# Kernel optimization log

Measured on AMD Instinct MI355X. Metric: run time of the kernel, lower is better.

The kernel has to match this reference:

```python
import jax, jax.numpy as jnp
import numpy as np

N = 50000      # nodes
E = 600000     # edges
F_IN = 9       # atom features
H = 128        # hidden dim
G = 2048       # graphs in batch
EPS = 1e-5     # batchnorm eps


def setup_inputs() -> dict:
    key = jax.random.key(0)
    ks = jax.random.split(key, 24)

    def lin(k, i, o):
        return (jax.random.normal(k, (i, o), jnp.float32) / np.sqrt(i).astype(np.float32))

    x = jax.random.normal(ks[0], (N, F_IN), jnp.float32)
    edge_index = jax.random.randint(ks[1], (2, E), 0, N, dtype=jnp.int32)
    # deterministic sorted graph assignment: every graph non-empty (~24 nodes each)
    batch = ((jnp.arange(N, dtype=jnp.int32) * G) // N).astype(jnp.int32)

    return {
        "x": x, "edge_index": edge_index, "batch": batch,
        "W0": lin(ks[2], F_IN, H), "b0": jnp.zeros((H,), jnp.float32),
        "g0": jnp.ones((H,), jnp.float32), "be0": jnp.zeros((H,), jnp.float32),
        "W1": lin(ks[3], H, H), "b1": jnp.zeros((H,), jnp.float32),
        "g1": jnp.ones((H,), jnp.float32), "be1": jnp.zeros((H,), jnp.float32),
        "W2": lin(ks[4], H, H), "b2": jnp.zeros((H,), jnp.float32),
        "g2": jnp.ones((H,), jnp.float32), "be2": jnp.zeros((H,), jnp.float32),
        "fc1_w": lin(ks[5], 2 * H, H), "fc1_b": jnp.zeros((H,), jnp.float32),
        "fc2_w": lin(ks[6], H, H // 2), "fc2_b": jnp.zeros((H // 2,), jnp.float32),
        "out_w": lin(ks[7], H // 2, 5), "out_b": jnp.zeros((5,), jnp.float32),
    }


def _gcn_conv(x, src, dst, W, b):
    # PyG GCNConv: add self-loops, symmetric deg^-1/2 normalization.
    h = x @ W                                   # [N, H_out]
    deg = jax.ops.segment_sum(jnp.ones((E,), h.dtype), dst, num_segments=N) + 1.0
    dis = jax.lax.rsqrt(deg)                    # deg^-1/2 incl. self-loop
    coef = dis[src] * dis[dst]                  # [E]
    agg = jax.ops.segment_sum(h[src] * coef[:, None], dst, num_segments=N)
    agg = agg + h * (dis * dis)[:, None]        # self-loop messages
    return agg + b


def _bn_relu(x, g, b):
    m = jnp.mean(x, axis=0)
    v = jnp.mean(jnp.square(x - m), axis=0)     # biased variance (torch BN)
    return jax.nn.relu((x - m) * jax.lax.rsqrt(v + EPS) * g + b)


def reference(x, edge_index, batch,
              W0, b0, g0, be0, W1, b1, g1, be1, W2, b2, g2, be2,
              fc1_w, fc1_b, fc2_w, fc2_b, out_w, out_b):
    src, dst = edge_index[0], edge_index[1]

    h = _bn_relu(_gcn_conv(x, src, dst, W0, b0), g0, be0)
    h = _bn_relu(_gcn_conv(h, src, dst, W1, b1), g1, be1)
    h = _bn_relu(_gcn_conv(h, src, dst, W2, b2), g2, be2)

    counts = jax.ops.segment_sum(jnp.ones((N,), h.dtype), batch, num_segments=G)
    x_mean = jax.ops.segment_sum(h, batch, num_segments=G) / jnp.maximum(counts, 1.0)[:, None]
    x_max = jax.ops.segment_max(h, batch, num_segments=G)

    z = jnp.concatenate([x_mean, x_max], axis=1)        # [G, 2H]
    z = jax.nn.relu(z @ fc1_w + fc1_b)
    z = jax.nn.relu(z @ fc2_w + fc2_b)
    return z @ out_w + out_b                            # [G, 5]
```

## Files before the change

### kernel.cpp

```cpp
#include <hip/hip_runtime.h>
#include <hip/hip_bf16.h>

#define N_NODES 50000
#define N_EDGES 600000
#define F_INX 9
#define HD 128
#define G_GRAPHS 2048
#define BN_EPS 1e-5f

#define SCAN_CHUNK 1024
#define SCAN_BLOCKS ((N_NODES + SCAN_CHUNK - 1) / SCAN_CHUNK)
#define BN_SLICES 16
#define BN_LAYER_F (BN_SLICES * 256)

typedef __bf16 bf16x8 __attribute__((ext_vector_type(8)));
typedef float f32x4 __attribute__((ext_vector_type(4)));

__device__ inline unsigned short f2bf(float f) {
    union { float f; unsigned u; } v;
    v.f = f;
    unsigned r = v.u + 0x7fff + ((v.u >> 16) & 1);
    return (unsigned short)(r >> 16);
}
__device__ inline float asf(unsigned u) {
    union { unsigned u; float f; } v;
    v.u = u;
    return v.f;
}

__global__ void k_zero(int* __restrict__ cnt, float* __restrict__ bnacc) {
    int i = blockIdx.x * blockDim.x + threadIdx.x;
    if (i < N_NODES) cnt[i] = 0;
    if (i < 3 * BN_LAYER_F) bnacc[i] = 0.0f;
}

__global__ void k_count(const int* __restrict__ dst, int* __restrict__ cnt) {
    int e = blockIdx.x * blockDim.x + threadIdx.x;
    if (e < N_EDGES) atomicAdd(&cnt[dst[e]], 1);
}

__global__ void k_scanA(const int* __restrict__ cnt, int* __restrict__ blocksum) {
    __shared__ int red[256];
    int b = blockIdx.x, t = threadIdx.x;
    int idx = b * SCAN_CHUNK + t * 4;
    int s = 0;
    if (idx + 3 < N_NODES) {
        int4 v = *(const int4*)(cnt + idx);
        s = v.x + v.y + v.z + v.w;
    }
    red[t] = s;
    __syncthreads();
    for (int off = 128; off > 0; off >>= 1) {
        if (t < off) red[t] += red[t + off];
        __syncthreads();
    }
    if (t == 0) blocksum[b] = red[0];
}

__global__ void k_scanB(const int* __restrict__ blocksum, int* __restrict__ blockoff) {
    int t = threadIdx.x;
    int v = (t < SCAN_BLOCKS) ? blocksum[t] : 0;
    int incl = v;
    for (int off = 1; off < 64; off <<= 1) {
        int u = __shfl_up(incl, off, 64);
        if (t >= off) incl += u;
    }
    if (t < SCAN_BLOCKS) blockoff[t] = incl - v;
}

__global__ void k_scanC(const int* __restrict__ cnt, const int* __restrict__ blockoff,
                        int* __restrict__ rowptr, int* __restrict__ cursor,
                        float* __restrict__ dis) {
    __shared__ int pre[256];
    int b = blockIdx.x, t = threadIdx.x;
    int idx = b * SCAN_CHUNK + t * 4;
    int4 v = make_int4(0, 0, 0, 0);
    bool valid = (idx + 3 < N_NODES);
    if (valid) v = *(const int4*)(cnt + idx);
    int s = v.x + v.y + v.z + v.w;
    pre[t] = s;
    __syncthreads();
    for (int off = 1; off < 256; off <<= 1) {
        int u = (t >= off) ? pre[t - off] : 0;
        __syncthreads();
        pre[t] += u;
        __syncthreads();
    }
    if (valid) {
        int base = blockoff[b] + pre[t] - s;
        int4 rp;
        rp.x = base;
        rp.y = base + v.x;
        rp.z = rp.y + v.y;
        rp.w = rp.z + v.z;
        *(int4*)(rowptr + idx) = rp;
        *(int4*)(cursor + idx) = rp;
        float4 dv = make_float4(rsqrtf((float)v.x + 1.0f), rsqrtf((float)v.y + 1.0f),
                                rsqrtf((float)v.z + 1.0f), rsqrtf((float)v.w + 1.0f));
        *(float4*)(dis + idx) = dv;
    }
}

__global__ void k_scatter(const int* __restrict__ src, const int* __restrict__ dst,
                          const float* __restrict__ dis, int* __restrict__ cursor,
                          unsigned* __restrict__ ebuf) {
    int e = blockIdx.x * blockDim.x + threadIdx.x;
    if (e >= N_EDGES) return;
    int s = src[e], d = dst[e];
    int pos = atomicAdd(&cursor[d], 1);
    float coef = dis[s] * dis[d];
    ebuf[pos] = (unsigned)(s & 0xffff) | ((unsigned)f2bf(coef) << 16);
}

__global__ void k_wconv(const float* __restrict__ W, unsigned short* __restrict__ Wt) {
    int i = blockIdx.x * blockDim.x + threadIdx.x;
    int k = i >> 7, n = i & 127;
    Wt[n * HD + k] = f2bf(W[k * HD + n]);
}

template <int K, int NPB>
__global__ void k_lin0(const float* __restrict__ in, const float* __restrict__ W,
                       unsigned short* __restrict__ hout) {
    __shared__ float rows[NPB][K];
    int node0 = blockIdx.x * NPB;
    int c = threadIdx.x;
    for (int i = c; i < NPB * K; i += HD) {
        int n = i / K, k = i % K;
        int node = node0 + n;
        rows[n][k] = (node < N_NODES) ? in[(size_t)node * K + k] : 0.0f;
    }
    __syncthreads();
    float acc[NPB];
#pragma unroll
    for (int n = 0; n < NPB; ++n) acc[n] = 0.0f;
#pragma unroll
    for (int k = 0; k < K; ++k) {
        float w = W[k * HD + c];
#pragma unroll
        for (int n = 0; n < NPB; ++n) acc[n] += rows[n][k] * w;
    }
#pragma unroll
    for (int n = 0; n < NPB; ++n) {
        int node = node0 + n;
        if (node < N_NODES) hout[(size_t)node * HD + c] = f2bf(acc[n]);
    }
}

#define LIN_ROWS 64
#define ATS 136

__global__ __launch_bounds__(256, 3) void k_linear_mfma(
        const float* __restrict__ in, const unsigned short* __restrict__ Wt,
        const float* __restrict__ bnp,
        const float* __restrict__ gam, const float* __restrict__ bet,
        unsigned short* __restrict__ hout) {
    __shared__ __align__(16) unsigned short At[LIN_ROWS][ATS];
    __shared__ __align__(16) unsigned short Bt[HD][ATS];
    __shared__ float sc_s[HD], sh_s[HD];
    int node0 = blockIdx.x * LIN_ROWS;
    int t = threadIdx.x;

    if (t < HD) {
        float s = 0.0f, q = 0.0f;
#pragma unroll
        for (int i = 0; i < BN_SLICES; ++i) {
            s += bnp[i * 256 + t];
            q += bnp[i * 256 + 128 + t];
        }
        const float inv_n = 1.0f / (float)N_NODES;
        float m = s * inv_n;
        float v = q * inv_n - m * m;
        float sc = gam[t] * rsqrtf(v + BN_EPS);
        sc_s[t] = sc;
        sh_s[t] = bet[t] - m * sc;
    }
    __syncthreads();

    for (int i = t; i < LIN_ROWS * 32; i += 256) {
        int r = i >> 5;
        int k4 = (i & 31) * 4;
        int node = node0 + r;
        float4 v = make_float4(0.f, 0.f, 0.f, 0.f);
        if (node < N_NODES) v = *(const float4*)(in + (size_t)node * HD + k4);
        ushort4 o;
        o.x = f2bf(fmaxf(0.f, v.x * sc_s[k4 + 0] + sh_s[k4 + 0]));
        o.y = f2bf(fmaxf(0.f, v.y * sc_s[k4 + 1] + sh_s[k4 + 1]));
        o.z = f2bf(fmaxf(0.f, v.z * sc_s[k4 + 2] + sh_s[k4 + 2]));
        o.w = f2bf(fmaxf(0.f, v.w * sc_s[k4 + 3] + sh_s[k4 + 3]));
        *(ushort4*)&At[r][k4] = o;
    }
    for (int c = t; c < HD * 16; c += 256) {
        int n = c >> 4, k8 = (c & 15) * 8;
        *(ushort4*)&Bt[n][k8] = *(const ushort4*)(Wt + (size_t)n * HD + k8);
        *(ushort4*)&Bt[n][k8 + 4] = *(const ushort4*)(Wt + (size_t)n * HD + k8 + 4);
    }
    __syncthreads();

    int w = t >> 6, l = t & 63;
    int quad = l >> 4, lc = l & 15;
    int arow = w * 16 + lc;
    int koff = quad * 8;

    f32x4 acc[8];
#pragma unroll
    for (int nt = 0; nt < 8; ++nt) acc[nt] = (f32x4){0.f, 0.f, 0.f, 0.f};

#pragma unroll
    for (int kb = 0; kb < HD; kb += 32) {
        bf16x8 af = *(const bf16x8*)&At[arow][kb + koff];
#pragma unroll
        for (int nt = 0; nt < 8; ++nt) {
            bf16x8 bfg = *(const bf16x8*)&Bt[nt * 16 + lc][kb + koff];
            acc[nt] = __builtin_amdgcn_mfma_f32_16x16x32_bf16(af, bfg, acc[nt], 0, 0, 0);
        }
    }

    int node_base = node0 + w * 16 + quad * 4;
#pragma unroll
    for (int nt = 0; nt < 8; ++nt) {
#pragma unroll
        for (int r = 0; r < 4; ++r) {
            int node = node_base + r;
            if (node < N_NODES)
                hout[(size_t)node * HD + nt * 16 + lc] = f2bf(acc[nt][r]);
        }
    }
}

__global__ __launch_bounds__(256, 8) void k_gather(
        const int* __restrict__ rowptr, const int* __restrict__ cnt,
        const unsigned* __restrict__ ebuf, const unsigned short* __restrict__ h,
        const float* __restrict__ dis, float* __restrict__ agg,
        float* __restrict__ bnp) {
    __shared__ float redS[4][256];
    __shared__ float redQ[4][256];
    int wv = threadIdx.x >> 6;
    int lane = threadIdx.x & 63;
    int node = __builtin_amdgcn_readfirstlane(blockIdx.x * 4 + wv);
    const unsigned* h32 = (const unsigned*)h;

    int start = rowptr[node];
    int deg = cnt[node];
    float d = dis[node];
    unsigned sv = h32[(size_t)node * 64 + lane];
    float dd = d * d;
    float acc0 = asf(sv << 16) * dd;
    float acc1 = asf(sv & 0xffff0000u) * dd;

    int e = start, end = start + deg;
    for (; e + 4 <= end; e += 4) {
        unsigned r0 = ebuf[e], r1 = ebuf[e + 1], r2 = ebuf[e + 2], r3 = ebuf[e + 3];
        unsigned hv0 = h32[(size_t)(r0 & 0xffffu) * 64 + lane];
        unsigned hv1 = h32[(size_t)(r1 & 0xffffu) * 64 + lane];
        unsigned hv2 = h32[(size_t)(r2 & 0xffffu) * 64 + lane];
        unsigned hv3 = h32[(size_t)(r3 & 0xffffu) * 64 + lane];
        float c0 = asf(r0 & 0xffff0000u), c1 = asf(r1 & 0xffff0000u);
        float c2 = asf(r2 & 0xffff0000u), c3 = asf(r3 & 0xffff0000u);
        acc0 += asf(hv0 << 16) * c0;
        acc1 += asf(hv0 & 0xffff0000u) * c0;
        acc0 += asf(hv1 << 16) * c1;
        acc1 += asf(hv1 & 0xffff0000u) * c1;
        acc0 += asf(hv2 << 16) * c2;
        acc1 += asf(hv2 & 0xffff0000u) * c2;
        acc0 += asf(hv3 << 16) * c3;
        acc1 += asf(hv3 & 0xffff0000u) * c3;
    }
    for (; e < end; ++e) {
        unsigned r = ebuf[e];
        unsigned hv = h32[(size_t)(r & 0xffffu) * 64 + lane];
        float cf = asf(r & 0xffff0000u);
        acc0 += asf(hv << 16) * cf;
        acc1 += asf(hv & 0xffff0000u) * cf;
    }

    ((float2*)agg)[(size_t)node * 64 + lane] = make_float2(acc0, acc1);

    redS[wv][2 * lane] = acc0;
    redS[wv][2 * lane + 1] = acc1;
    redQ[wv][2 * lane] = acc0 * acc0;
    redQ[wv][2 * lane + 1] = acc1 * acc1;
    __syncthreads();
    int t = threadIdx.x;
    int ch = t & 127;
    int which = t >> 7;
    float val;
    if (which == 0)
        val = redS[0][ch] + redS[1][ch] + redS[2][ch] + redS[3][ch];
    else
        val = redQ[0][ch] + redQ[1][ch] + redQ[2][ch] + redQ[3][ch];
    int slice = blockIdx.x & (BN_SLICES - 1);
    atomicAdd(&bnp[slice * 256 + which * 128 + ch], val);
}

__global__ void k_head(const float* __restrict__ agg, const float* __restrict__ bnp,
                       const float* __restrict__ gam, const float* __restrict__ bet,
                       const float* __restrict__ fc1_w, const float* __restrict__ fc1_b,
                       const float* __restrict__ fc2_w, const float* __restrict__ fc2_b,
                       const float* __restrict__ out_w, const float* __restrict__ out_b,
                       float* __restrict__ out) {
    __shared__ float z[2 * HD];
    __shared__ float z1[HD];
    __shared__ float z2[64];
    int g = blockIdx.x, c = threadIdx.x;
    float s = 0.0f, q = 0.0f;
#pragma unroll
    for (int i = 0; i < BN_SLICES; ++i) {
        s += bnp[i * 256 + c];
        q += bnp[i * 256 + 128 + c];
    }
    const float inv_n = 1.0f / (float)N_NODES;
    float m = s * inv_n;
    float v = q * inv_n - m * m;
    float sc = gam[c] * rsqrtf(v + BN_EPS);
    float sh = bet[c] - m * sc;
    int start = (g * N_NODES + G_GRAPHS - 1) / G_GRAPHS;
    int end = ((g + 1) * N_NODES + G_GRAPHS - 1) / G_GRAPHS;
    float sm = 0.0f, mx = 0.0f;
    for (int n = start; n < end; ++n) {
        float val = fmaxf(0.0f, agg[(size_t)n * HD + c] * sc + sh);
        sm += val;
        mx = fmaxf(mx, val);
    }
    z[c] = sm / (float)(end - start);
    z[HD + c] = mx;
    __syncthreads();
    float a1 = fc1_b[c];
#pragma unroll 8
    for (int k = 0; k < 2 * HD; ++k) a1 += z[k] * fc1_w[k * HD + c];
    z1[c] = fmaxf(a1, 0.0f);
    __syncthreads();
    if (c < 64) {
        float a2 = fc2_b[c];
#pragma unroll 8
        for (int k = 0; k < HD; ++k) a2 += z1[k] * fc2_w[k * 64 + c];
        z2[c] = fmaxf(a2, 0.0f);
    }
    __syncthreads();
    if (c < 5) {
        float a3 = out_b[c];
#pragma unroll
        for (int k = 0; k < 64; ++k) a3 += z2[k] * out_w[k * 5 + c];
        out[(size_t)g * 5 + c] = a3;
    }
}

extern "C" void kernel_launch(void* const* d_in, const int* in_sizes, int n_in,
                              void* d_out, int out_size, void* d_ws, size_t ws_size,
                              hipStream_t stream) {
    const float* x = (const float*)d_in[0];
    const int* edge_index = (const int*)d_in[1];
    const float* W0 = (const float*)d_in[3];
    const float* g0 = (const float*)d_in[5];
    const float* be0 = (const float*)d_in[6];
    const float* W1 = (const float*)d_in[7];
    const float* g1 = (const float*)d_in[9];
    const float* be1 = (const float*)d_in[10];
    const float* W2 = (const float*)d_in[11];
    const float* g2 = (const float*)d_in[13];
    const float* be2 = (const float*)d_in[14];
    const float* fc1_w = (const float*)d_in[15];
    const float* fc1_b = (const float*)d_in[16];
    const float* fc2_w = (const float*)d_in[17];
    const float* fc2_b = (const float*)d_in[18];
    const float* out_w = (const float*)d_in[19];
    const float* out_b = (const float*)d_in[20];
    float* out = (float*)d_out;

    const int* src = edge_index;
    const int* dst = edge_index + N_EDGES;

    char* ws = (char*)d_ws;
    size_t off = 0;
    auto alloc = [&](size_t bytes) {
        char* p = ws + off;
        off += (bytes + 255) & ~(size_t)255;
        return p;
    };
    int* cnt = (int*)alloc(N_NODES * 4);
    int* rowptr = (int*)alloc(N_NODES * 4);
    int* cursor = (int*)alloc(N_NODES * 4);
    float* dis = (float*)alloc(N_NODES * 4);
    int* blocksum = (int*)alloc(SCAN_BLOCKS * 4);
    int* blockoff = (int*)alloc(SCAN_BLOCKS * 4);
    unsigned* ebuf = (unsigned*)alloc((size_t)N_EDGES * 4);
    unsigned short* hbuf = (unsigned short*)alloc((size_t)N_NODES * HD * 2);
    float* aggbuf = (float*)alloc((size_t)N_NODES * HD * 4);
    float* bnacc = (float*)alloc((size_t)3 * BN_LAYER_F * 4);
    unsigned short* wt1 = (unsigned short*)alloc(HD * HD * 2);
    unsigned short* wt2 = (unsigned short*)alloc(HD * HD * 2);
    (void)ws_size;

    float* bnp0 = bnacc + 0 * BN_LAYER_F;
    float* bnp1 = bnacc + 1 * BN_LAYER_F;
    float* bnp2 = bnacc + 2 * BN_LAYER_F;

    k_zero<<<(N_NODES + 255) / 256, 256, 0, stream>>>(cnt, bnacc);
    k_count<<<(N_EDGES + 255) / 256, 256, 0, stream>>>(dst, cnt);
    k_scanA<<<SCAN_BLOCKS, 256, 0, stream>>>(cnt, blocksum);
    k_scanB<<<1, 64, 0, stream>>>(blocksum, blockoff);
    k_scanC<<<SCAN_BLOCKS, 256, 0, stream>>>(cnt, blockoff, rowptr, cursor, dis);
    k_scatter<<<(N_EDGES + 255) / 256, 256, 0, stream>>>(src, dst, dis, cursor, ebuf);
    k_wconv<<<HD * HD / 256, 256, 0, stream>>>(W1, wt1);
    k_wconv<<<HD * HD / 256, 256, 0, stream>>>(W2, wt2);

    const int LIN_GRID = (N_NODES + LIN_ROWS - 1) / LIN_ROWS;
    const int GATHER_GRID = N_NODES / 4;

    k_lin0<F_INX, 8><<<(N_NODES + 7) / 8, HD, 0, stream>>>(x, W0, hbuf);
    k_gather<<<GATHER_GRID, 256, 0, stream>>>(rowptr, cnt, ebuf, hbuf, dis, aggbuf, bnp0);
    k_linear_mfma<<<LIN_GRID, 256, 0, stream>>>(aggbuf, wt1, bnp0, g0, be0, hbuf);
    k_gather<<<GATHER_GRID, 256, 0, stream>>>(rowptr, cnt, ebuf, hbuf, dis, aggbuf, bnp1);
    k_linear_mfma<<<LIN_GRID, 256, 0, stream>>>(aggbuf, wt2, bnp1, g1, be1, hbuf);
    k_gather<<<GATHER_GRID, 256, 0, stream>>>(rowptr, cnt, ebuf, hbuf, dis, aggbuf, bnp2);

    k_head<<<G_GRAPHS, HD, 0, stream>>>(aggbuf, bnp2, g2, be2, fc1_w, fc1_b,
                                        fc2_w, fc2_b, out_w, out_b, out);
}
```

Baseline: 329.6 us.

## Store aggregates as bf16, pre-swizzle weights into MFMA fragment order, fuse setup kernels

The gather kernel now writes the aggregated features as packed bf16 instead of fp32, which halves the traffic of the largest intermediate read by the linear and head kernels. Weights are pre-permuted into MFMA fragment order so the linear kernel reads B fragments straight from global memory, dropping the shared B tile and raising the occupancy hint. Zeroing, weight conversion and the first layer's linear are merged into one preamble kernel, and the block-offset scan is folded into scanC, which cuts several launches. The cost is extra bf16 rounding of pre-BN activations, which could slightly change accuracy.

```diff
diff --git a/kernel.cpp b/kernel.cpp
--- a/kernel.cpp
+++ b/kernel.cpp
@@ -13,6 +13,12 @@
 #define BN_SLICES 16
 #define BN_LAYER_F (BN_SLICES * 256)
 
+#define NB_LIN0 3125
+#define NB_WCONV 16
+#define NB_ZCNT 196
+#define NB_ZBN 48
+#define NB_PRE (NB_LIN0 + NB_WCONV + NB_ZCNT + NB_ZBN)
+
 typedef __bf16 bf16x8 __attribute__((ext_vector_type(8)));
 typedef float f32x4 __attribute__((ext_vector_type(4)));
 
@@ -27,11 +33,57 @@
     v.u = u;
     return v.f;
 }
-
-__global__ void k_zero(int* __restrict__ cnt, float* __restrict__ bnacc) {
-    int i = blockIdx.x * blockDim.x + threadIdx.x;
-    if (i < N_NODES) cnt[i] = 0;
-    if (i < 3 * BN_LAYER_F) bnacc[i] = 0.0f;
+__device__ inline unsigned packbf(float a, float b) {
+    return (unsigned)f2bf(a) | ((unsigned)f2bf(b) << 16);
+}
+
+__global__ __launch_bounds__(256) void k_preamble(
+        const float* __restrict__ x, const float* __restrict__ W0,
+        const float* __restrict__ W1, const float* __restrict__ W2,
+        int* __restrict__ cnt, float* __restrict__ bnacc,
+        unsigned short* __restrict__ wf1, unsigned short* __restrict__ wf2,
+        unsigned short* __restrict__ hout) {
+    int b = blockIdx.x, t = threadIdx.x;
+    if (b < NB_LIN0) {
+        __shared__ float rows[16][F_INX];
+        int node0 = b * 16;
+        for (int i = t; i < 16 * F_INX; i += 256)
+            rows[i / F_INX][i % F_INX] = x[(size_t)node0 * F_INX + i];
+        __syncthreads();
+        int half = t >> 7, c = t & 127;
+        float acc[8];
+#pragma unroll
+        for (int n = 0; n < 8; ++n) acc[n] = 0.0f;
+#pragma unroll
+        for (int k = 0; k < F_INX; ++k) {
+            float w = W0[k * HD + c];
+#pragma unroll
+            for (int n = 0; n < 8; ++n) acc[n] += rows[half * 8 + n][k] * w;
+        }
+#pragma unroll
+        for (int n = 0; n < 8; ++n)
+            hout[(size_t)(node0 + half * 8 + n) * HD + c] = f2bf(acc[n]);
+    } else if (b < NB_LIN0 + NB_WCONV) {
+        int bw = b - NB_LIN0;
+        const float* W = (bw < 8) ? W1 : W2;
+        unsigned short* Wf = (bw < 8) ? wf1 : wf2;
+        int triple = (bw & 7) * 256 + t;
+        int kb = triple >> 9;
+        int rest = triple & 511;
+        int nt = rest >> 6;
+        int l = rest & 63;
+        int quad = l >> 4, lc = l & 15;
+#pragma unroll
+        for (int j = 0; j < 8; ++j)
+            Wf[(size_t)triple * 8 + j] =
+                f2bf(W[(size_t)(kb * 32 + quad * 8 + j) * HD + nt * 16 + lc]);
+    } else if (b < NB_LIN0 + NB_WCONV + NB_ZCNT) {
+        int idx = (b - NB_LIN0 - NB_WCONV) * 256 + t;
+        if (idx < N_NODES) cnt[idx] = 0;
+    } else {
+        int idx = (b - NB_LIN0 - NB_WCONV - NB_ZCNT) * 256 + t;
+        if (idx < 3 * BN_LAYER_F) bnacc[idx] = 0.0f;
+    }
 }
 
 __global__ void k_count(const int* __restrict__ dst, int* __restrict__ cnt) {
@@ -57,22 +109,21 @@
     if (t == 0) blocksum[b] = red[0];
 }
 
-__global__ void k_scanB(const int* __restrict__ blocksum, int* __restrict__ blockoff) {
-    int t = threadIdx.x;
-    int v = (t < SCAN_BLOCKS) ? blocksum[t] : 0;
-    int incl = v;
-    for (int off = 1; off < 64; off <<= 1) {
-        int u = __shfl_up(incl, off, 64);
-        if (t >= off) incl += u;
-    }
-    if (t < SCAN_BLOCKS) blockoff[t] = incl - v;
-}
-
-__global__ void k_scanC(const int* __restrict__ cnt, const int* __restrict__ blockoff,
+__global__ void k_scanC(const int* __restrict__ cnt, const int* __restrict__ blocksum,
                         int* __restrict__ rowptr, int* __restrict__ cursor,
                         float* __restrict__ dis) {
     __shared__ int pre[256];
+    __shared__ int myoff_s;
     int b = blockIdx.x, t = threadIdx.x;
+    if (t < 64) {
+        int v = (t < SCAN_BLOCKS) ? blocksum[t] : 0;
+        int incl = v;
+        for (int off = 1; off < 64; off <<= 1) {
+            int u = __shfl_up(incl, off, 64);
+            if (t >= off) incl += u;
+        }
+        if (t == b) myoff_s = incl - v;
+    }
     int idx = b * SCAN_CHUNK + t * 4;
     int4 v = make_int4(0, 0, 0, 0);
     bool valid = (idx + 3 < N_NODES);
@@ -87,7 +138,7 @@
         __syncthreads();
     }
     if (valid) {
-        int base = blockoff[b] + pre[t] - s;
+        int base = myoff_s + pre[t] - s;
         int4 rp;
         rp.x = base;
         rp.y = base + v.x;
@@ -112,50 +163,14 @@
     ebuf[pos] = (unsigned)(s & 0xffff) | ((unsigned)f2bf(coef) << 16);
 }
 
-__global__ void k_wconv(const float* __restrict__ W, unsigned short* __restrict__ Wt) {
-    int i = blockIdx.x * blockDim.x + threadIdx.x;
-    int k = i >> 7, n = i & 127;
-    Wt[n * HD + k] = f2bf(W[k * HD + n]);
-}
-
-template <int K, int NPB>
-__global__ void k_lin0(const float* __restrict__ in, const float* __restrict__ W,
-                       unsigned short* __restrict__ hout) {
-    __shared__ float rows[NPB][K];
-    int node0 = blockIdx.x * NPB;
-    int c = threadIdx.x;
-    for (int i = c; i < NPB * K; i += HD) {
-        int n = i / K, k = i % K;
-        int node = node0 + n;
-        rows[n][k] = (node < N_NODES) ? in[(size_t)node * K + k] : 0.0f;
-    }
-    __syncthreads();
-    float acc[NPB];
-#pragma unroll
-    for (int n = 0; n < NPB; ++n) acc[n] = 0.0f;
-#pragma unroll
-    for (int k = 0; k < K; ++k) {
-        float w = W[k * HD + c];
-#pragma unroll
-        for (int n = 0; n < NPB; ++n) acc[n] += rows[n][k] * w;
-    }
-#pragma unroll
-    for (int n = 0; n < NPB; ++n) {
-        int node = node0 + n;
-        if (node < N_NODES) hout[(size_t)node * HD + c] = f2bf(acc[n]);
-    }
-}
-
 #define LIN_ROWS 64
 #define ATS 136
 
-__global__ __launch_bounds__(256, 3) void k_linear_mfma(
-        const float* __restrict__ in, const unsigned short* __restrict__ Wt,
-        const float* __restrict__ bnp,
-        const float* __restrict__ gam, const float* __restrict__ bet,
-        unsigned short* __restrict__ hout) {
+__global__ __launch_bounds__(256, 4) void k_linear_mfma(
+        const unsigned* __restrict__ agg32, const unsigned short* __restrict__ Wf,
+        const float* __restrict__ bnp, const float* __restrict__ gam,
+        const float* __restrict__ bet, unsigned short* __restrict__ hout) {
     __shared__ __align__(16) unsigned short At[LIN_ROWS][ATS];
-    __shared__ __align__(16) unsigned short Bt[HD][ATS];
     __shared__ float sc_s[HD], sh_s[HD];
     int node0 = blockIdx.x * LIN_ROWS;
     int t = threadIdx.x;
@@ -176,23 +191,24 @@
     }
     __syncthreads();
 
-    for (int i = t; i < LIN_ROWS * 32; i += 256) {
-        int r = i >> 5;
-        int k4 = (i & 31) * 4;
+    for (int i = t; i < LIN_ROWS * 16; i += 256) {
+        int r = i >> 4;
+        int c8 = (i & 15) * 8;
         int node = node0 + r;
-        float4 v = make_float4(0.f, 0.f, 0.f, 0.f);
-        if (node < N_NODES) v = *(const float4*)(in + (size_t)node * HD + k4);
-        ushort4 o;
-        o.x = f2bf(fmaxf(0.f, v.x * sc_s[k4 + 0] + sh_s[k4 + 0]));
-        o.y = f2bf(fmaxf(0.f, v.y * sc_s[k4 + 1] + sh_s[k4 + 1]));
-        o.z = f2bf(fmaxf(0.f, v.z * sc_s[k4 + 2] + sh_s[k4 + 2]));
-        o.w = f2bf(fmaxf(0.f, v.w * sc_s[k4 + 3] + sh_s[k4 + 3]));
-        *(ushort4*)&At[r][k4] = o;
-    }
-    for (int c = t; c < HD * 16; c += 256) {
-        int n = c >> 4, k8 = (c & 15) * 8;
-        *(ushort4*)&Bt[n][k8] = *(const ushort4*)(Wt + (size_t)n * HD + k8);
-        *(ushort4*)&Bt[n][k8 + 4] = *(const ushort4*)(Wt + (size_t)n * HD + k8 + 4);
+        uint4 u = make_uint4(0, 0, 0, 0);
+        if (node < N_NODES) u = *(const uint4*)(agg32 + (size_t)node * 64 + c8 / 2);
+        unsigned uu[4] = {u.x, u.y, u.z, u.w};
+        unsigned short o[8];
+#pragma unroll
+        for (int j = 0; j < 4; ++j) {
+            float e = asf(uu[j] << 16);
+            float od = asf(uu[j] & 0xffff0000u);
+            int ce = c8 + 2 * j, co = ce + 1;
+            o[2 * j] = f2bf(fmaxf(0.f, e * sc_s[ce] + sh_s[ce]));
+            o[2 * j + 1] = f2bf(fmaxf(0.f, od * sc_s[co] + sh_s[co]));
+        }
+        *(ushort4*)&At[r][c8] = *(ushort4*)&o[0];
+        *(ushort4*)&At[r][c8 + 4] = *(ushort4*)&o[4];
     }
     __syncthreads();
 
@@ -206,11 +222,11 @@
     for (int nt = 0; nt < 8; ++nt) acc[nt] = (f32x4){0.f, 0.f, 0.f, 0.f};
 
 #pragma unroll
-    for (int kb = 0; kb < HD; kb += 32) {
-        bf16x8 af = *(const bf16x8*)&At[arow][kb + koff];
+    for (int kb = 0; kb < 4; ++kb) {
+        bf16x8 af = *(const bf16x8*)&At[arow][kb * 32 + koff];
 #pragma unroll
         for (int nt = 0; nt < 8; ++nt) {
-            bf16x8 bfg = *(const bf16x8*)&Bt[nt * 16 + lc][kb + koff];
+            bf16x8 bfg = *(const bf16x8*)&Wf[(size_t)(((kb * 8) + nt) * 64 + l) * 8];
             acc[nt] = __builtin_amdgcn_mfma_f32_16x16x32_bf16(af, bfg, acc[nt], 0, 0, 0);
         }
     }
@@ -230,7 +246,7 @@
 __global__ __launch_bounds__(256, 8) void k_gather(
         const int* __restrict__ rowptr, const int* __restrict__ cnt,
         const unsigned* __restrict__ ebuf, const unsigned short* __restrict__ h,
-        const float* __restrict__ dis, float* __restrict__ agg,
+        const float* __restrict__ dis, unsigned* __restrict__ agg32,
         float* __restrict__ bnp) {
     __shared__ float redS[4][256];
     __shared__ float redQ[4][256];
@@ -273,7 +289,7 @@
         acc1 += asf(hv & 0xffff0000u) * cf;
     }
 
-    ((float2*)agg)[(size_t)node * 64 + lane] = make_float2(acc0, acc1);
+    agg32[(size_t)node * 64 + lane] = packbf(acc0, acc1);
 
     redS[wv][2 * lane] = acc0;
     redS[wv][2 * lane + 1] = acc1;
@@ -292,12 +308,12 @@
     atomicAdd(&bnp[slice * 256 + which * 128 + ch], val);
 }
 
-__global__ void k_head(const float* __restrict__ agg, const float* __restrict__ bnp,
-                       const float* __restrict__ gam, const float* __restrict__ bet,
-                       const float* __restrict__ fc1_w, const float* __restrict__ fc1_b,
-                       const float* __restrict__ fc2_w, const float* __restrict__ fc2_b,
-                       const float* __restrict__ out_w, const float* __restrict__ out_b,
-                       float* __restrict__ out) {
+__global__ void k_head(const unsigned short* __restrict__ agg16,
+                       const float* __restrict__ bnp, const float* __restrict__ gam,
+                       const float* __restrict__ bet, const float* __restrict__ fc1_w,
+                       const float* __restrict__ fc1_b, const float* __restrict__ fc2_w,
+                       const float* __restrict__ fc2_b, const float* __restrict__ out_w,
+                       const float* __restrict__ out_b, float* __restrict__ out) {
     __shared__ float z[2 * HD];
     __shared__ float z1[HD];
     __shared__ float z2[64];
@@ -317,7 +333,8 @@
     int end = ((g + 1) * N_NODES + G_GRAPHS - 1) / G_GRAPHS;
     float sm = 0.0f, mx = 0.0f;
     for (int n = start; n < end; ++n) {
-        float val = fmaxf(0.0f, agg[(size_t)n * HD + c] * sc + sh);
+        float raw = asf((unsigned)agg16[(size_t)n * HD + c] << 16);
+        float val = fmaxf(0.0f, raw * sc + sh);
         sm += val;
         mx = fmaxf(mx, val);
     }
@@ -381,38 +398,33 @@
     int* cursor = (int*)alloc(N_NODES * 4);
     float* dis = (float*)alloc(N_NODES * 4);
     int* blocksum = (int*)alloc(SCAN_BLOCKS * 4);
-    int* blockoff = (int*)alloc(SCAN_BLOCKS * 4);
     unsigned* ebuf = (unsigned*)alloc((size_t)N_EDGES * 4);
     unsigned short* hbuf = (unsigned short*)alloc((size_t)N_NODES * HD * 2);
-    float* aggbuf = (float*)alloc((size_t)N_NODES * HD * 4);
+    unsigned* aggbuf = (unsigned*)alloc((size_t)N_NODES * 64 * 4);
     float* bnacc = (float*)alloc((size_t)3 * BN_LAYER_F * 4);
-    unsigned short* wt1 = (unsigned short*)alloc(HD * HD * 2);
-    unsigned short* wt2 = (unsigned short*)alloc(HD * HD * 2);
+    unsigned short* wf1 = (unsigned short*)alloc(HD * HD * 2);
+    unsigned short* wf2 = (unsigned short*)alloc(HD * HD * 2);
     (void)ws_size;
 
     float* bnp0 = bnacc + 0 * BN_LAYER_F;
     float* bnp1 = bnacc + 1 * BN_LAYER_F;
     float* bnp2 = bnacc + 2 * BN_LAYER_F;
 
-    k_zero<<<(N_NODES + 255) / 256, 256, 0, stream>>>(cnt, bnacc);
+    k_preamble<<<NB_PRE, 256, 0, stream>>>(x, W0, W1, W2, cnt, bnacc, wf1, wf2, hbuf);
     k_count<<<(N_EDGES + 255) / 256, 256, 0, stream>>>(dst, cnt);
     k_scanA<<<SCAN_BLOCKS, 256, 0, stream>>>(cnt, blocksum);
-    k_scanB<<<1, 64, 0, stream>>>(blocksum, blockoff);
-    k_scanC<<<SCAN_BLOCKS, 256, 0, stream>>>(cnt, blockoff, rowptr, cursor, dis);
+    k_scanC<<<SCAN_BLOCKS, 256, 0, stream>>>(cnt, blocksum, rowptr, cursor, dis);
     k_scatter<<<(N_EDGES + 255) / 256, 256, 0, stream>>>(src, dst, dis, cursor, ebuf);
-    k_wconv<<<HD * HD / 256, 256, 0, stream>>>(W1, wt1);
-    k_wconv<<<HD * HD / 256, 256, 0, stream>>>(W2, wt2);
 
     const int LIN_GRID = (N_NODES + LIN_ROWS - 1) / LIN_ROWS;
     const int GATHER_GRID = N_NODES / 4;
 
-    k_lin0<F_INX, 8><<<(N_NODES + 7) / 8, HD, 0, stream>>>(x, W0, hbuf);
     k_gather<<<GATHER_GRID, 256, 0, stream>>>(rowptr, cnt, ebuf, hbuf, dis, aggbuf, bnp0);
-    k_linear_mfma<<<LIN_GRID, 256, 0, stream>>>(aggbuf, wt1, bnp0, g0, be0, hbuf);
+    k_linear_mfma<<<LIN_GRID, 256, 0, stream>>>(aggbuf, wf1, bnp0, g0, be0, hbuf);
     k_gather<<<GATHER_GRID, 256, 0, stream>>>(rowptr, cnt, ebuf, hbuf, dis, aggbuf, bnp1);
-    k_linear_mfma<<<LIN_GRID, 256, 0, stream>>>(aggbuf, wt2, bnp1, g1, be1, hbuf);
+    k_linear_mfma<<<LIN_GRID, 256, 0, stream>>>(aggbuf, wf2, bnp1, g1, be1, hbuf);
     k_gather<<<GATHER_GRID, 256, 0, stream>>>(rowptr, cnt, ebuf, hbuf, dis, aggbuf, bnp2);
 
-    k_head<<<G_GRAPHS, HD, 0, stream>>>(aggbuf, bnp2, g2, be2, fc1_w, fc1_b,
-                                        fc2_w, fc2_b, out_w, out_b, out);
-}
+    k_head<<<G_GRAPHS, HD, 0, stream>>>((const unsigned short*)aggbuf, bnp2, g2, be2,
+                                        fc1_w, fc1_b, fc2_w, fc2_b, out_w, out_b, out);
+}
```

Result: no change. 330.4 us (+0.2%).
